# Kernel optimization log

Hardware: AMD Instinct MI355X
Metric: run time of the kernel (lower is better)

Reference implementation:

```python
import jax, jax.numpy as jnp
import numpy as np

N = 30000      # entities
E = 200000     # KG triples
E_ALL = 400000 # full-graph edges
R = 500        # relations
EH = 300       # e_hidden
RH = 100       # r_hidden
H = 8          # GAT / R2E heads
H_E2R = 2      # E2R heads: int(softmax(head_selector).sum()+1) == 2 always
EPS = 1e-16    # torch_geometric softmax eps


def _seg_softmax(logits, idx, num):
    # logits: [E, heads]; segment-wise stable softmax over edges grouped by idx
    m = jax.ops.segment_max(logits, idx, num_segments=num)
    ex = jnp.exp(logits - m[idx])
    s = jax.ops.segment_sum(ex, idx, num_segments=num)
    return ex / (s[idx] + EPS)


def _gcn(x, ei):
    j, i = ei[0], ei[1]
    deg = jax.ops.segment_sum(jnp.ones(ei.shape[1], x.dtype), i, num_segments=N)
    dis = jnp.where(deg > 0, deg ** -0.5, 0.0)
    norm = dis[j] * dis[i]                                        # [E_all]
    agg = jax.ops.segment_sum(norm[:, None] * x[j], i, num_segments=N)
    return jax.nn.relu(agg)


def _highway(x1, x2, w, b):
    gate = jax.nn.sigmoid(x1 @ w.T + b)
    return gate * x2 + (1.0 - gate) * x1


def setup_inputs() -> dict:
    key = jax.random.key(0)
    ks = jax.random.split(key, 20)
    f = jnp.float32
    inp = {
        'x_e': jax.random.normal(ks[0], (N, EH), f),
        'edge_index': jax.random.randint(ks[1], (2, E), 0, N),
        'rel': jax.random.randint(ks[2], (E,), 0, R),
        'edge_index_all': jax.random.randint(ks[3], (2, E_ALL), 0, N),
        'rel_all': jax.random.randint(ks[4], (E_ALL,), 0, R),
        # Highway layers
        'hw1_w': jax.random.normal(ks[5], (EH, EH), f) / np.sqrt(EH),
        'hw1_b': jnp.zeros((EH,), f),
        'hw2_w': jax.random.normal(ks[6], (EH, EH), f) / np.sqrt(EH),
        'hw2_b': jnp.zeros((EH,), f),
        # E2R (only first H_E2R heads are ever used)
        'e2r_wh': jax.random.normal(ks[7], (RH, EH), f) / np.sqrt(EH),
        'e2r_wt': jax.random.normal(ks[8], (RH, EH), f) / np.sqrt(EH),
        'e2r_ah': jax.random.normal(ks[9], (H_E2R, RH), f) / np.sqrt(RH),
        'e2r_at': jax.random.normal(ks[10], (H_E2R, RH), f) / np.sqrt(RH),
        # R2E
        'r2e_ah': jax.random.normal(ks[11], (H, EH), f) / np.sqrt(EH),
        'r2e_at': jax.random.normal(ks[12], (H, EH), f) / np.sqrt(EH),
        'r2e_ar': jax.random.normal(ks[13], (H, RH), f) / np.sqrt(RH),
        # GAT over e_hidden + 2*r_hidden = 500
        'gat_ai': jax.random.normal(ks[14], (H, EH + 2 * RH), f) / np.sqrt(EH + 2 * RH),
        'gat_aj': jax.random.normal(ks[15], (H, EH + 2 * RH), f) / np.sqrt(EH + 2 * RH),
    }
    return inp


def reference(x_e, edge_index, rel, edge_index_all, rel_all,
              hw1_w, hw1_b, hw2_w, hw2_b,
              e2r_wh, e2r_wt, e2r_ah, e2r_at,
              r2e_ah, r2e_at, r2e_ar, gat_ai, gat_aj):
    lrelu = jax.nn.leaky_relu  # slope 0.01, matches torch default

    # --- two GCN + Highway blocks (dropout = identity at eval) ---
    x = _highway(x_e, _gcn(x_e, edge_index_all), hw1_w, hw1_b)
    x = _highway(x, _gcn(x, edge_index_all), hw2_w, hw2_b)

    h_idx, t_idx = edge_index[0], edge_index[1]

    # --- E2R: entity -> relation (2 heads; spmm sum over heads folded into alpha sum) ---
    xh = x @ e2r_wh.T                        # [N, RH]
    xt = x @ e2r_wt.T                        # [N, RH]
    e1 = (xh @ e2r_ah.T)[h_idx] + (xt @ e2r_at.T)[t_idx]   # [E, H_E2R]
    a1 = _seg_softmax(lrelu(e1), rel, R)
    xr_h = jax.ops.segment_sum(a1.sum(1)[:, None] * xh[h_idx], rel, num_segments=R)
    e2 = (xt @ e2r_ah.T)[h_idx] + (xh @ e2r_at.T)[t_idx]
    a2 = _seg_softmax(lrelu(e2), rel, R)
    xr_t = jax.ops.segment_sum(a2.sum(1)[:, None] * xt[t_idx], rel, num_segments=R)
    x_r = (xr_h + xr_t) / H_E2R / 2.0        # [R, RH]

    # --- R2E: relation -> entity (8 heads) ---
    se_h = x @ r2e_ah.T                      # [N, H]
    se_t = x @ r2e_at.T
    sr = x_r @ r2e_ar.T                      # [R, H]
    a_h = _seg_softmax(lrelu(se_h[h_idx] + sr[rel]), h_idx, N)
    a_t = _seg_softmax(lrelu(se_t[t_idx] + sr[rel]), t_idx, N)
    xr_rel = x_r[rel]                        # [E, RH]
    xe_h = jax.ops.segment_sum(a_h.sum(1)[:, None] * xr_rel, h_idx, num_segments=N) / H
    xe_t = jax.ops.segment_sum(a_t.sum(1)[:, None] * xr_rel, t_idx, num_segments=N) / H
    x2 = jnp.concatenate([x, xe_h, xe_t], axis=1)          # [N, EH+2*RH]

    # --- GAT over full graph (8 heads) ---
    j_a, i_a = edge_index_all[0], edge_index_all[1]
    e_ij = (x2 @ gat_ai.T)[i_a] + (x2 @ gat_aj.T)[j_a]     # [E_all, H]
    al = _seg_softmax(lrelu(e_ij), i_a, N)
    x_gat = jax.ops.segment_sum(al.sum(1)[:, None] * x2[j_a], i_a, num_segments=N) / H

    return jnp.concatenate([x2, x_gat], axis=1)            # [N, 2*(EH+2*RH)]
```

## Files before the change

### kernel.cpp

```cpp
#include <hip/hip_runtime.h>
#include <math.h>

constexpr int N_    = 30000;
constexpr int E_    = 200000;
constexpr int EALL_ = 400000;
constexpr int R_    = 500;
constexpr int EH_   = 300;
constexpr int RH_   = 100;
constexpr int X2D_  = 500;
constexpr int OUTD_ = 1000;
constexpr int LD4   = OUTD_/4;
constexpr int EH4   = EH_/4;
constexpr int RH4   = RH_/4;
constexpr int NC_   = 16;
constexpr int XBS_  = 320;
constexpr int XEBS_ = 200;
constexpr int KP_   = 320;
constexpr int NBR_  = 64;
constexpr int PERB_ = (E_ + NBR_ - 1)/NBR_;

typedef __attribute__((ext_vector_type(4))) float f32x4;
typedef __attribute__((ext_vector_type(8))) short s16x8;

__device__ __forceinline__ float lrelu_(float v){ return v > 0.f ? v : 0.01f*v; }
__device__ __forceinline__ float sig_(float z){ return 1.f/(1.f + expf(-z)); }
__device__ __forceinline__ unsigned short f2bf_(float f){
  unsigned int u = __float_as_uint(f);
  unsigned int r = (u + 0x7FFFu + ((u >> 16) & 1u)) >> 16;
  return (unsigned short)r;
}
__device__ __forceinline__ float bf2f_(unsigned short h){
  return __uint_as_float(((unsigned int)h) << 16);
}

__global__ void k_count3(const int* __restrict__ ia,
                         const int* __restrict__ hi, const int* __restrict__ ti,
                         int* cd, int* ch, int* ct){
  int idx = blockIdx.x*blockDim.x + threadIdx.x;
  if (idx < EALL_) { atomicAdd(&cd[ia[idx]], 1); return; }
  idx -= EALL_;
  if (idx < E_) { atomicAdd(&ch[hi[idx]], 1); return; }
  idx -= E_;
  if (idx < E_) { atomicAdd(&ct[ti[idx]], 1); return; }
}

__global__ void k_scan3(const int* c0, int* o0, int L0,
                        const int* c1, int* o1, int L1,
                        const int* c2, int* o2, int L2,
                        float* __restrict__ dis){
  const int* c; int* o; int L;
  switch (blockIdx.x){
    case 0: c=c0; o=o0; L=L0; break;
    case 1: c=c1; o=o1; L=L1; break;
    default: c=c2; o=o2; L=L2; break;
  }
  __shared__ int sums[256];
  int t = threadIdx.x;
  int chunk = (L + 255) / 256;
  int s = min(t*chunk, L), e = min(s + chunk, L);
  int acc = 0;
  for (int i = s; i < e; ++i) acc += c[i];
  sums[t] = acc;
  __syncthreads();
  for (int off = 1; off < 256; off <<= 1) {
    int v = (t >= off) ? sums[t - off] : 0;
    __syncthreads();
    sums[t] += v;
    __syncthreads();
  }
  int run = t ? sums[t-1] : 0;
  for (int i = s; i < e; ++i) {
    o[i] = run; run += c[i];
    if (blockIdx.x == 0) dis[i] = (c[i] > 0) ? rsqrtf((float)c[i]) : 0.f;
  }
  if (t == 255) o[L] = sums[255];
}

__global__ void k_scatter3(const int* __restrict__ ja, const int* __restrict__ ia,
                           const int* __restrict__ rel, const int* __restrict__ hi,
                           const int* __restrict__ ti,
                           const int* od, const int* oh, const int* ot,
                           int* curd, int* curh, int* curt,
                           const float* __restrict__ dis,
                           int* j_dest, float* wj,
                           int* relh, int* relt){
  int idx = blockIdx.x*blockDim.x + threadIdx.x;
  if (idx < EALL_){
    int e = idx, s = ia[e];
    int p = od[s] + atomicAdd(&curd[s], 1);
    int j = ja[e];
    j_dest[p] = j; wj[p] = dis[j]; return;
  }
  idx -= EALL_;
  if (idx < E_){
    int e = idx, s = hi[e];
    int p = oh[s] + atomicAdd(&curh[s], 1);
    relh[p] = rel[e]; return;
  }
  idx -= E_;
  if (idx < E_){
    int e = idx, s = ti[e];
    int p = ot[s] + atomicAdd(&curt[s], 1);
    relt[p] = rel[e]; return;
  }
}

__global__ void k_relhist(const int* __restrict__ rel, int* __restrict__ H){
  __shared__ int h[R_];
  int b = blockIdx.x, tid = threadIdx.x;
  for (int i = tid; i < R_; i += 256) h[i] = 0;
  __syncthreads();
  int s = b*PERB_, e = min(s + PERB_, E_);
  for (int i = s + tid; i < e; i += 256) atomicAdd(&h[rel[i]], 1);
  __syncthreads();
  for (int i = tid; i < R_; i += 256) H[b*R_ + i] = h[i];
}

__global__ void k_relscan(int* __restrict__ H, int* __restrict__ off_rel){
  __shared__ int tot[R_];
  int tid = threadIdx.x;
  for (int r = tid; r < R_; r += 256){
    int acc = 0;
    for (int b = 0; b < NBR_; ++b){ int v = H[b*R_ + r]; H[b*R_ + r] = acc; acc += v; }
    tot[r] = acc;
  }
  __syncthreads();
  if (tid == 0){
    int run = 0;
    for (int r = 0; r < R_; ++r){ off_rel[r] = run; run += tot[r]; }
    off_rel[R_] = run;
  }
  __syncthreads();
  for (int r = tid; r < R_; r += 256){
    int o = off_rel[r];
    for (int b = 0; b < NBR_; ++b) H[b*R_ + r] += o;
  }
}

__global__ void k_relscatter(const int* __restrict__ rel, const int* __restrict__ hi,
                             const int* __restrict__ ti, const int* __restrict__ H,
                             int* __restrict__ hr, int* __restrict__ tr){
  __shared__ int cur[R_];
  int b = blockIdx.x, tid = threadIdx.x;
  for (int i = tid; i < R_; i += 256) cur[i] = H[b*R_ + i];
  __syncthreads();
  int s = b*PERB_, e = min(s + PERB_, E_);
  for (int i = s + tid; i < e; i += 256){
    int r = rel[i];
    int p = atomicAdd(&cur[r], 1);
    hr[p] = hi[i]; tr[p] = ti[i];
  }
}

__global__ void k_pack_x(const float4* __restrict__ X, int ldx4,
                         unsigned short* __restrict__ xb){
  int idx = blockIdx.x*blockDim.x + threadIdx.x;
  if (idx >= N_*80) return;
  int n = idx / 80, c = idx - n*80;
  ushort4 o = make_ushort4(0,0,0,0);
  if (c < EH4){
    float4 v = X[(size_t)n*ldx4 + c];
    o.x = f2bf_(v.x); o.y = f2bf_(v.y); o.z = f2bf_(v.z); o.w = f2bf_(v.w);
  }
  *reinterpret_cast<ushort4*>(&xb[(size_t)n*XBS_ + c*4]) = o;
}

__global__ void k_pack_w(const float* __restrict__ W, int Nn,
                         unsigned short* __restrict__ out){
  int idx = blockIdx.x*blockDim.x + threadIdx.x;
  if (idx >= Nn*KP_) return;
  int n = idx / KP_, k = idx - n*KP_;
  out[idx] = (k < EH_) ? f2bf_(W[(size_t)n*EH_ + k]) : (unsigned short)0;
}

__global__ void k_pack_wcat(const float* __restrict__ wh, const float* __restrict__ wt,
                            unsigned short* __restrict__ out){
  int idx = blockIdx.x*blockDim.x + threadIdx.x;
  if (idx >= 200*KP_) return;
  int n = idx / KP_, k = idx - n*KP_;
  unsigned short v = 0;
  if (k < EH_) v = f2bf_((n < 100) ? wh[(size_t)n*EH_ + k] : wt[(size_t)(n-100)*EH_ + k]);
  out[idx] = v;
}

__global__ __launch_bounds__(256) void k_gemm_mfma(
    const unsigned short* __restrict__ Ab,
    const unsigned short* __restrict__ Wb,
    float* __restrict__ C, int ldc, int M, int Nn){
  constexpr int WS = 328;
  constexpr int AS = 40;
  __shared__ unsigned short Ws[64*WS];
  __shared__ unsigned short As[128*AS];
  int tid = threadIdx.x;
  int lane = tid & 63, wave = tid >> 6;
  int wm = wave & 1, wn = wave >> 1;
  int m0 = blockIdx.x*128, n0 = blockIdx.y*64;

  for (int c = tid; c < 64*(KP_/8); c += 256){
    int n = c / (KP_/8), k8 = (c % (KP_/8))*8;
    s16x8 v = {0,0,0,0,0,0,0,0};
    if (n0 + n < Nn)
      v = *reinterpret_cast<const s16x8*>(&Wb[(size_t)(n0+n)*KP_ + k8]);
    *reinterpret_cast<s16x8*>(&Ws[n*WS + k8]) = v;
  }

  f32x4 acc[4][2] = {};
  int kf = (lane >> 4)*8;
  int rA = lane & 15;
  for (int k0 = 0; k0 < KP_; k0 += 32){
    __syncthreads();
    for (int c = tid; c < 128*4; c += 256){
      int r = c >> 2, k8 = (c & 3)*8;
      s16x8 v = {0,0,0,0,0,0,0,0};
      if (m0 + r < M)
        v = *reinterpret_cast<const s16x8*>(&Ab[(size_t)(m0+r)*XBS_ + k0 + k8]);
      *reinterpret_cast<s16x8*>(&As[r*AS + k8]) = v;
    }
    __syncthreads();
    s16x8 afr[4], bfr[2];
    #pragma unroll
    for (int mf = 0; mf < 4; ++mf)
      afr[mf] = *reinterpret_cast<const s16x8*>(&As[(wm*64 + mf*16 + rA)*AS + kf]);
    #pragma unroll
    for (int nf = 0; nf < 2; ++nf)
      bfr[nf] = *reinterpret_cast<const s16x8*>(&Ws[(wn*32 + nf*16 + rA)*WS + k0 + kf]);
    #pragma unroll
    for (int mf = 0; mf < 4; ++mf)
      #pragma unroll
      for (int nf = 0; nf < 2; ++nf)
        acc[mf][nf] = __builtin_amdgcn_mfma_f32_16x16x32_bf16(afr[mf], bfr[nf], acc[mf][nf], 0, 0, 0);
  }
  int col0 = n0 + wn*32 + (lane & 15);
  int rbase = m0 + wm*64 + (lane >> 4)*4;
  #pragma unroll
  for (int mf = 0; mf < 4; ++mf){
    #pragma unroll
    for (int nf = 0; nf < 2; ++nf){
      int col = col0 + nf*16;
      if (col < Nn){
        #pragma unroll
        for (int r = 0; r < 4; ++r){
          int row = rbase + mf*16 + r;
          if (row < M) C[(size_t)row*ldc + col] = acc[mf][nf][r];
        }
      }
    }
  }
}

__global__ void k_gcn4(const int* __restrict__ off, const int* __restrict__ jd,
                       const float* __restrict__ wj, const float* __restrict__ dis,
                       const unsigned short* __restrict__ xb, float4* __restrict__ Y){
  __shared__ int js[64];
  __shared__ float ws[64];
  int n = blockIdx.x, lane = threadIdx.x;
  int s = off[n], t = off[n+1];
  bool two = lane < (EH4 - 64);
  float4 a0 = make_float4(0.f,0.f,0.f,0.f);
  float4 a1 = make_float4(0.f,0.f,0.f,0.f);
  for (int base = s; base < t; base += 64){
    int m = min(64, t - base);
    __syncthreads();
    if (lane < m){ js[lane] = jd[base+lane]; ws[lane] = wj[base+lane]; }
    __syncthreads();
    int q = 0;
    for (; q + 1 < m; q += 2){
      size_t r0 = (size_t)js[q]*XBS_, r1 = (size_t)js[q+1]*XBS_;
      float w0 = ws[q], w1 = ws[q+1];
      ushort4 u0 = *reinterpret_cast<const ushort4*>(&xb[r0 + lane*4]);
      ushort4 u1 = *reinterpret_cast<const ushort4*>(&xb[r1 + lane*4]);
      a0.x += w0*bf2f_(u0.x) + w1*bf2f_(u1.x);
      a0.y += w0*bf2f_(u0.y) + w1*bf2f_(u1.y);
      a0.z += w0*bf2f_(u0.z) + w1*bf2f_(u1.z);
      a0.w += w0*bf2f_(u0.w) + w1*bf2f_(u1.w);
      if (two){
        ushort4 v0 = *reinterpret_cast<const ushort4*>(&xb[r0 + 256 + lane*4]);
        ushort4 v1 = *reinterpret_cast<const ushort4*>(&xb[r1 + 256 + lane*4]);
        a1.x += w0*bf2f_(v0.x) + w1*bf2f_(v1.x);
        a1.y += w0*bf2f_(v0.y) + w1*bf2f_(v1.y);
        a1.z += w0*bf2f_(v0.z) + w1*bf2f_(v1.z);
        a1.w += w0*bf2f_(v0.w) + w1*bf2f_(v1.w);
      }
    }
    if (q < m){
      size_t r0 = (size_t)js[q]*XBS_;
      float w0 = ws[q];
      ushort4 u0 = *reinterpret_cast<const ushort4*>(&xb[r0 + lane*4]);
      a0.x += w0*bf2f_(u0.x); a0.y += w0*bf2f_(u0.y);
      a0.z += w0*bf2f_(u0.z); a0.w += w0*bf2f_(u0.w);
      if (two){
        ushort4 v0 = *reinterpret_cast<const ushort4*>(&xb[r0 + 256 + lane*4]);
        a1.x += w0*bf2f_(v0.x); a1.y += w0*bf2f_(v0.y);
        a1.z += w0*bf2f_(v0.z); a1.w += w0*bf2f_(v0.w);
      }
    }
  }
  float dn = dis[n];
  float4 r;
  r.x = fmaxf(dn*a0.x, 0.f); r.y = fmaxf(dn*a0.y, 0.f);
  r.z = fmaxf(dn*a0.z, 0.f); r.w = fmaxf(dn*a0.w, 0.f);
  Y[(size_t)n*EH4 + lane] = r;
  if (two){
    r.x = fmaxf(dn*a1.x, 0.f); r.y = fmaxf(dn*a1.y, 0.f);
    r.z = fmaxf(dn*a1.z, 0.f); r.w = fmaxf(dn*a1.w, 0.f);
    Y[(size_t)n*EH4 + 64 + lane] = r;
  }
}

__global__ void k_highway3(const float4* __restrict__ Xold, int ldo4,
                           const float4* __restrict__ Y, const float4* __restrict__ G,
                           const float* __restrict__ b,
                           float4* __restrict__ Xn, unsigned short* __restrict__ xbb){
  int idx = blockIdx.x*blockDim.x + threadIdx.x;
  if (idx >= N_*EH4) return;
  int n = idx / EH4, f = idx - n*EH4;
  float4 g4 = G[idx];
  float4 b4 = reinterpret_cast<const float4*>(b)[f];
  float4 y4 = Y[idx];
  float4 xo = Xold[(size_t)n*ldo4 + f];
  float4 r;
  float gx;
  gx = sig_(g4.x + b4.x); r.x = gx*y4.x + (1.f-gx)*xo.x;
  gx = sig_(g4.y + b4.y); r.y = gx*y4.y + (1.f-gx)*xo.y;
  gx = sig_(g4.z + b4.z); r.z = gx*y4.z + (1.f-gx)*xo.z;
  gx = sig_(g4.w + b4.w); r.w = gx*y4.w + (1.f-gx)*xo.w;
  Xn[(size_t)n*LD4 + f] = r;
  ushort4 o;
  o.x = f2bf_(r.x); o.y = f2bf_(r.y); o.z = f2bf_(r.z); o.w = f2bf_(r.w);
  *reinterpret_cast<ushort4*>(&xbb[(size_t)n*XBS_ + f*4]) = o;
}

__global__ void k_pproj(const float* __restrict__ xhxt,
                        const float* __restrict__ ah, const float* __restrict__ at,
                        float4* __restrict__ pht){
  int n = blockIdx.x*blockDim.x + threadIdx.x;
  if (n >= N_) return;
  float a0=0,a1=0,b0=0,b1=0,c0=0,c1=0,d0=0,d1=0;
  const float* xh = xhxt + (size_t)n*200;
  const float* xt = xh + 100;
  for (int f = 0; f < RH_; ++f) {
    float vh = xh[f], vt = xt[f];
    float w0 = ah[f], w1 = ah[RH_+f], u0 = at[f], u1 = at[RH_+f];
    a0 += vh*w0; a1 += vh*w1;
    b0 += vt*u0; b1 += vt*u1;
    c0 += vt*w0; c1 += vt*w1;
    d0 += vh*u0; d1 += vh*u1;
  }
  pht[(size_t)n*2]     = make_float4(a0, a1, c0, c1);
  pht[(size_t)n*2 + 1] = make_float4(b0, b1, d0, d1);
}

__global__ void k_fold_rel2(const int* __restrict__ off,
                            const int* __restrict__ hr, const int* __restrict__ tr,
                            const float4* __restrict__ pht,
                            float* __restrict__ s1p, float* __restrict__ s2p){
  __shared__ float4 redm[4];
  __shared__ float4 reds[4];
  int r = blockIdx.x;
  int tid = threadIdx.x, lane = tid & 63, w = tid >> 6;
  int s = off[r], e = off[r+1];
  float4 mx = make_float4(-1e30f,-1e30f,-1e30f,-1e30f);
  for (int p = s + tid; p < e; p += 256){
    float4 ph = pht[(size_t)hr[p]*2];
    float4 pt = pht[(size_t)tr[p]*2 + 1];
    mx.x = fmaxf(mx.x, lrelu_(ph.x + pt.x));
    mx.y = fmaxf(mx.y, lrelu_(ph.y + pt.y));
    mx.z = fmaxf(mx.z, lrelu_(ph.z + pt.z));
    mx.w = fmaxf(mx.w, lrelu_(ph.w + pt.w));
  }
  #pragma unroll
  for (int o = 1; o < 64; o <<= 1){
    mx.x = fmaxf(mx.x, __shfl_xor(mx.x, o));
    mx.y = fmaxf(mx.y, __shfl_xor(mx.y, o));
    mx.z = fmaxf(mx.z, __shfl_xor(mx.z, o));
    mx.w = fmaxf(mx.w, __shfl_xor(mx.w, o));
  }
  if (lane == 0) redm[w] = mx;
  __syncthreads();
  float4 m;
  m.x = fmaxf(fmaxf(redm[0].x, redm[1].x), fmaxf(redm[2].x, redm[3].x));
  m.y = fmaxf(fmaxf(redm[0].y, redm[1].y), fmaxf(redm[2].y, redm[3].y));
  m.z = fmaxf(fmaxf(redm[0].z, redm[1].z), fmaxf(redm[2].z, redm[3].z));
  m.w = fmaxf(fmaxf(redm[0].w, redm[1].w), fmaxf(redm[2].w, redm[3].w));
  float4 sm = make_float4(0.f,0.f,0.f,0.f);
  for (int p = s + tid; p < e; p += 256){
    float4 ph = pht[(size_t)hr[p]*2];
    float4 pt = pht[(size_t)tr[p]*2 + 1];
    sm.x += expf(lrelu_(ph.x + pt.x) - m.x);
    sm.y += expf(lrelu_(ph.y + pt.y) - m.y);
    sm.z += expf(lrelu_(ph.z + pt.z) - m.z);
    sm.w += expf(lrelu_(ph.w + pt.w) - m.w);
  }
  #pragma unroll
  for (int o = 1; o < 64; o <<= 1){
    sm.x += __shfl_xor(sm.x, o);
    sm.y += __shfl_xor(sm.y, o);
    sm.z += __shfl_xor(sm.z, o);
    sm.w += __shfl_xor(sm.w, o);
  }
  if (lane == 0) reds[w] = sm;
  __syncthreads();
  float4 sv;
  sv.x = reds[0].x + reds[1].x + reds[2].x + reds[3].x;
  sv.y = reds[0].y + reds[1].y + reds[2].y + reds[3].y;
  sv.z = reds[0].z + reds[1].z + reds[2].z + reds[3].z;
  sv.w = reds[0].w + reds[1].w + reds[2].w + reds[3].w;
  float4 inv;
  inv.x = 1.f/(sv.x + 1e-16f); inv.y = 1.f/(sv.y + 1e-16f);
  inv.z = 1.f/(sv.z + 1e-16f); inv.w = 1.f/(sv.w + 1e-16f);
  for (int p = s + tid; p < e; p += 256){
    float4 ph = pht[(size_t)hr[p]*2];
    float4 pt = pht[(size_t)tr[p]*2 + 1];
    s1p[p] = expf(lrelu_(ph.x + pt.x) - m.x)*inv.x + expf(lrelu_(ph.y + pt.y) - m.y)*inv.y;
    s2p[p] = expf(lrelu_(ph.z + pt.z) - m.z)*inv.z + expf(lrelu_(ph.w + pt.w) - m.w)*inv.w;
  }
}

__global__ void k_fold_ht2(const int* __restrict__ offh, const int* __restrict__ offt,
                           const int* __restrict__ relh, const int* __restrict__ relt,
                           const float* __restrict__ st16, const float* __restrict__ sr8,
                           float* __restrict__ shp, float* __restrict__ stp){
  int w = threadIdx.x >> 6, lane = threadIdx.x & 63;
  int n = blockIdx.x*2 + (w >> 1);
  if (n >= N_) return;
  int side = w & 1;
  const int* off = side ? offt : offh;
  const int* rl  = side ? relt : relh;
  float* op = side ? stp : shp;
  int k = lane & 7, g = lane >> 3;
  float cst = st16[(size_t)n*16 + side*8 + k];
  int s = off[n], e = off[n+1];
  float m = -1e30f;
  for (int p = s + g; p < e; p += 8)
    m = fmaxf(m, lrelu_(cst + sr8[(size_t)rl[p]*8 + k]));
  #pragma unroll
  for (int o = 8; o < 64; o <<= 1) m = fmaxf(m, __shfl_xor(m, o));
  float sum = 0.f;
  for (int p = s + g; p < e; p += 8)
    sum += expf(lrelu_(cst + sr8[(size_t)rl[p]*8 + k]) - m);
  #pragma unroll
  for (int o = 8; o < 64; o <<= 1) sum += __shfl_xor(sum, o);
  float inv = 1.f / (sum + 1e-16f);
  for (int p = s + g; p < e; p += 8){
    float t = expf(lrelu_(cst + sr8[(size_t)rl[p]*8 + k]) - m) * inv;
    #pragma unroll
    for (int o = 1; o < 8; o <<= 1) t += __shfl_xor(t, o);
    if (k == 0) op[p] = t;
  }
}

__global__ void k_fold_gat2(const int* __restrict__ off, const int* __restrict__ jd,
                            const float* __restrict__ gg16, float* __restrict__ agp){
  int w = threadIdx.x >> 6, lane = threadIdx.x & 63;
  int n = blockIdx.x*4 + w;
  if (n >= N_) return;
  int k = lane & 7, g = lane >> 3;
  float cst = gg16[(size_t)n*16 + k];
  int s = off[n], e = off[n+1];
  float m = -1e30f;
  for (int p = s + g; p < e; p += 8)
    m = fmaxf(m, lrelu_(cst + gg16[(size_t)jd[p]*16 + 8 + k]));
  #pragma unroll
  for (int o = 8; o < 64; o <<= 1) m = fmaxf(m, __shfl_xor(m, o));
  float sum = 0.f;
  for (int p = s + g; p < e; p += 8)
    sum += expf(lrelu_(cst + gg16[(size_t)jd[p]*16 + 8 + k]) - m);
  #pragma unroll
  for (int o = 8; o < 64; o <<= 1) sum += __shfl_xor(sum, o);
  float inv = 1.f / (sum + 1e-16f);
  for (int p = s + g; p < e; p += 8){
    float t = expf(lrelu_(cst + gg16[(size_t)jd[p]*16 + 8 + k]) - m) * inv;
    #pragma unroll
    for (int o = 1; o < 8; o <<= 1) t += __shfl_xor(t, o);
    if (k == 0) agp[p] = t;
  }
}

__global__ void k_e2r_agg3(const int* __restrict__ off,
                           const int* __restrict__ hr, const int* __restrict__ tr,
                           const float* __restrict__ s1p, const float* __restrict__ s2p,
                           const float4* __restrict__ xhxt4, float4* __restrict__ xr_part){
  int r = blockIdx.x, c = blockIdx.y;
  int lane = threadIdx.x;
  int side = lane >> 5, fl = lane & 31;
  int s = off[r], e = off[r+1];
  int len = e - s;
  int per = (len + NC_ - 1)/NC_;
  int cs = s + c*per, ce = min(cs + per, e);
  float4 acc = make_float4(0.f,0.f,0.f,0.f);
  if (fl < RH4){
    const int* idx = side ? tr : hr;
    const float* wv = side ? s2p : s1p;
    int fofs = side ? 25 + fl : fl;
    int p = cs;
    for (; p + 1 < ce; p += 2){
      float a0 = wv[p], a1 = wv[p+1];
      float4 v0 = xhxt4[(size_t)idx[p]*50 + fofs];
      float4 v1 = xhxt4[(size_t)idx[p+1]*50 + fofs];
      acc.x += a0*v0.x + a1*v1.x; acc.y += a0*v0.y + a1*v1.y;
      acc.z += a0*v0.z + a1*v1.z; acc.w += a0*v0.w + a1*v1.w;
    }
    if (p < ce){
      float a0 = wv[p];
      float4 v0 = xhxt4[(size_t)idx[p]*50 + fofs];
      acc.x += a0*v0.x; acc.y += a0*v0.y; acc.z += a0*v0.z; acc.w += a0*v0.w;
    }
  }
  float4 oth;
  oth.x = __shfl_xor(acc.x, 32); oth.y = __shfl_xor(acc.y, 32);
  oth.z = __shfl_xor(acc.z, 32); oth.w = __shfl_xor(acc.w, 32);
  if (side == 0 && fl < RH4){
    float4 o = make_float4(acc.x+oth.x, acc.y+oth.y, acc.z+oth.z, acc.w+oth.w);
    xr_part[((size_t)c*R_ + r)*RH4 + fl] = o;
  }
}

__global__ void k_e2r_red(const float4* __restrict__ xr_part, float4* __restrict__ xr4){
  int idx = blockIdx.x*blockDim.x + threadIdx.x;
  if (idx >= R_*RH4) return;
  float4 a = make_float4(0.f,0.f,0.f,0.f);
  #pragma unroll
  for (int c = 0; c < NC_; ++c){
    float4 v = xr_part[(size_t)c*R_*RH4 + idx];
    a.x += v.x; a.y += v.y; a.z += v.z; a.w += v.w;
  }
  xr4[idx] = make_float4(a.x*0.25f, a.y*0.25f, a.z*0.25f, a.w*0.25f);
}

__global__ void k_dots16(const float* __restrict__ X, int ldx, int K,
                         const float* __restrict__ wA, const float* __restrict__ wB,
                         float* __restrict__ out16, int M){
  __shared__ float xs[16][65];
  __shared__ float ws[16][65];
  int tid = threadIdx.x;
  int tx = tid & 15, ty = tid >> 4;
  int r0 = blockIdx.x*16;
  float acc = 0.f;
  for (int c0 = 0; c0 < K; c0 += 64){
    int cl = min(64, K - c0);
    #pragma unroll
    for (int i = 0; i < 4; ++i){
      int idx = tid + i*256;
      int r = idx >> 6, k = idx & 63;
      float xv = 0.f, wv = 0.f;
      if (k < cl && r0 + r < M) xv = X[(size_t)(r0+r)*ldx + c0 + k];
      if (k < cl) wv = (r < 8) ? wA[(size_t)r*K + c0 + k] : wB[(size_t)(r-8)*K + c0 + k];
      xs[r][k] = xv;
      ws[r][k] = wv;
    }
    __syncthreads();
    #pragma unroll
    for (int k = 0; k < 64; ++k) acc += xs[ty][k]*ws[tx][k];
    __syncthreads();
  }
  if (r0 + ty < M) out16[(size_t)(r0+ty)*16 + tx] = acc;
}

__global__ void k_sr(const float* __restrict__ xr, const float* __restrict__ ar,
                     float* __restrict__ sr8){
  int idx = blockIdx.x*blockDim.x + threadIdx.x;
  if (idx >= R_*8) return;
  int r = idx >> 3, h = idx & 7;
  float acc = 0.f;
  for (int k = 0; k < RH_; ++k) acc += xr[(size_t)r*RH_ + k]*ar[(size_t)h*RH_ + k];
  sr8[idx] = acc;
}

__global__ void k_r2e_agg2b(const int* __restrict__ offh, const int* __restrict__ offt,
                            const int* __restrict__ relh, const int* __restrict__ relt,
                            const float* __restrict__ shp, const float* __restrict__ stp,
                            const float4* __restrict__ xr4, float4* __restrict__ out,
                            unsigned short* __restrict__ xeb){
  int n = blockIdx.x;
  int side = threadIdx.x >> 6, lane = threadIdx.x & 63;
  const int* off = side ? offt : offh;
  const int* rr  = side ? relt : relh;
  const float* sp = side ? stp : shp;
  int s = off[n], e = off[n+1];
  if (lane >= RH4) return;
  float4 acc = make_float4(0.f,0.f,0.f,0.f);
  int p = s;
  for (; p + 1 < e; p += 2){
    float a0 = sp[p], a1 = sp[p+1];
    float4 v0 = xr4[(size_t)rr[p]*RH4 + lane];
    float4 v1 = xr4[(size_t)rr[p+1]*RH4 + lane];
    acc.x += a0*v0.x + a1*v1.x; acc.y += a0*v0.y + a1*v1.y;
    acc.z += a0*v0.z + a1*v1.z; acc.w += a0*v0.w + a1*v1.w;
  }
  if (p < e){
    float a0 = sp[p];
    float4 v0 = xr4[(size_t)rr[p]*RH4 + lane];
    acc.x += a0*v0.x; acc.y += a0*v0.y; acc.z += a0*v0.z; acc.w += a0*v0.w;
  }
  float4 o = make_float4(acc.x*0.125f, acc.y*0.125f, acc.z*0.125f, acc.w*0.125f);
  out[(size_t)n*LD4 + (side ? 100 : 75) + lane] = o;
  ushort4 ob;
  ob.x = f2bf_(o.x); ob.y = f2bf_(o.y); ob.z = f2bf_(o.z); ob.w = f2bf_(o.w);
  *reinterpret_cast<ushort4*>(&xeb[(size_t)n*XEBS_ + (side ? 100 : 0) + lane*4]) = ob;
}

__global__ void k_gat_agg4(const int* __restrict__ off, const int* __restrict__ jd,
                           const float* __restrict__ agp,
                           const unsigned short* __restrict__ xb,
                           const unsigned short* __restrict__ xeb,
                           float4* __restrict__ out){
  __shared__ int js[128];
  __shared__ float as_[128];
  int n = blockIdx.x, tid = threadIdx.x;
  int s = off[n], t = off[n+1];
  const unsigned short* tbl;
  size_t stride; int cofs;
  if (tid < 75){ tbl = xb;  stride = XBS_;  cofs = tid*4; }
  else         { tbl = xeb; stride = XEBS_; cofs = (tid-75)*4; }
  float4 acc = make_float4(0.f,0.f,0.f,0.f);
  for (int base = s; base < t; base += 128){
    int m = min(128, t - base);
    __syncthreads();
    if (tid < m){ js[tid] = jd[base+tid]; as_[tid] = agp[base+tid]; }
    __syncthreads();
    if (tid < 125){
      int q = 0;
      for (; q + 1 < m; q += 2){
        float a0 = as_[q], a1 = as_[q+1];
        ushort4 u0 = *reinterpret_cast<const ushort4*>(&tbl[(size_t)js[q]*stride + cofs]);
        ushort4 u1 = *reinterpret_cast<const ushort4*>(&tbl[(size_t)js[q+1]*stride + cofs]);
        acc.x += a0*bf2f_(u0.x) + a1*bf2f_(u1.x);
        acc.y += a0*bf2f_(u0.y) + a1*bf2f_(u1.y);
        acc.z += a0*bf2f_(u0.z) + a1*bf2f_(u1.z);
        acc.w += a0*bf2f_(u0.w) + a1*bf2f_(u1.w);
      }
      if (q < m){
        float a0 = as_[q];
        ushort4 u0 = *reinterpret_cast<const ushort4*>(&tbl[(size_t)js[q]*stride + cofs]);
        acc.x += a0*bf2f_(u0.x); acc.y += a0*bf2f_(u0.y);
        acc.z += a0*bf2f_(u0.z); acc.w += a0*bf2f_(u0.w);
      }
    }
  }
  if (tid < 125){
    float4 r = make_float4(acc.x*0.125f, acc.y*0.125f, acc.z*0.125f, acc.w*0.125f);
    out[(size_t)n*LD4 + 125 + tid] = r;
  }
}

static inline void gemm_mfma(const unsigned short* Ab, const unsigned short* Wb,
                             float* C, int ldc, int M, int Nn, hipStream_t st){
  dim3 g((M + 127)/128, (Nn + 63)/64);
  k_gemm_mfma<<<g, 256, 0, st>>>(Ab, Wb, C, ldc, M, Nn);
}

extern "C" void kernel_launch(void* const* d_in, const int* in_sizes, int n_in,
                              void* d_out, int out_size, void* d_ws, size_t ws_size,
                              hipStream_t stream) {
  const float* x_e   = (const float*)d_in[0];
  const int*   ei    = (const int*)d_in[1];
  const int*   rel   = (const int*)d_in[2];
  const int*   eia   = (const int*)d_in[3];
  const float* hw1_w = (const float*)d_in[5];
  const float* hw1_b = (const float*)d_in[6];
  const float* hw2_w = (const float*)d_in[7];
  const float* hw2_b = (const float*)d_in[8];
  const float* e2r_wh= (const float*)d_in[9];
  const float* e2r_wt= (const float*)d_in[10];
  const float* e2r_ah= (const float*)d_in[11];
  const float* e2r_at= (const float*)d_in[12];
  const float* r2e_ah= (const float*)d_in[13];
  const float* r2e_at= (const float*)d_in[14];
  const float* r2e_ar= (const float*)d_in[15];
  const float* gat_ai= (const float*)d_in[16];
  const float* gat_aj= (const float*)d_in[17];
  float* out = (float*)d_out;

  const int* hi = ei;
  const int* ti = ei + E_;
  const int* ja = eia;
  const int* ia = eia + EALL_;

  char* base = (char*)d_ws;
  size_t off = 0;
  auto alloc = [&](size_t bytes)->void*{
    void* p = base + off;
    off = (off + bytes + 255) & ~(size_t)255;
    return p;
  };

  size_t z0 = off;
  int* cnt_dest = (int*)alloc(N_*4);
  int* cur_dest = (int*)alloc(N_*4);
  int* cnt_h    = (int*)alloc(N_*4);
  int* cur_h    = (int*)alloc(N_*4);
  int* cnt_t    = (int*)alloc(N_*4);
  int* cur_t    = (int*)alloc(N_*4);
  size_t z1 = off;

  int* off_dest = (int*)alloc((N_+1)*4);
  int* off_rel  = (int*)alloc((R_+1)*4);
  int* off_h    = (int*)alloc((N_+1)*4);
  int* off_t    = (int*)alloc((N_+1)*4);
  int* Hrel     = (int*)alloc((size_t)NBR_*R_*4);
  int* j_dest   = (int*)alloc((size_t)EALL_*4);
  int* hr       = (int*)alloc((size_t)E_*4);
  int* tr       = (int*)alloc((size_t)E_*4);
  int* relh     = (int*)alloc((size_t)E_*4);
  int* relt     = (int*)alloc((size_t)E_*4);

  float* dis   = (float*)alloc(N_*4);
  float* wj    = (float*)alloc((size_t)EALL_*4);
  float* y     = (float*)alloc((size_t)N_*EH_*4);
  float* g     = (float*)alloc((size_t)N_*EH_*4);
  float* xhxt  = (float*)alloc((size_t)N_*200*4);
  float* pht   = (float*)alloc((size_t)N_*8*4);
  float* s1p   = (float*)alloc((size_t)E_*4);
  float* s2p   = (float*)alloc((size_t)E_*4);
  float* xr    = (float*)alloc((size_t)R_*RH_*4);
  float* xr_part=(float*)alloc((size_t)NC_*R_*RH_*4);
  float* st16  = (float*)alloc((size_t)N_*16*4);
  float* sr8   = (float*)alloc((size_t)R_*8*4);
  float* shp   = (float*)alloc((size_t)E_*4);
  float* stp   = (float*)alloc((size_t)E_*4);
  float* gg16  = (float*)alloc((size_t)N_*16*4);
  float* agp   = (float*)alloc((size_t)EALL_*4);
  unsigned short* xb  = (unsigned short*)alloc((size_t)N_*XBS_*2);
  unsigned short* xeb = (unsigned short*)alloc((size_t)N_*XEBS_*2);
  unsigned short* w1b = (unsigned short*)alloc((size_t)EH_*KP_*2);
  unsigned short* w2b = (unsigned short*)alloc((size_t)EH_*KP_*2);
  unsigned short* wcb = (unsigned short*)alloc((size_t)200*KP_*2);

  hipMemsetAsync(base + z0, 0, z1 - z0, stream);

  const int TB = 256;
  const int TOT = EALL_ + 2*E_;
  int gTOT  = (TOT + TB - 1)/TB;
  int gN    = (N_ + TB - 1)/TB;
  int gPKX  = (N_*80 + TB - 1)/TB;

  k_pack_w<<<(EH_*KP_ + TB - 1)/TB, TB, 0, stream>>>(hw1_w, EH_, w1b);
  k_pack_w<<<(EH_*KP_ + TB - 1)/TB, TB, 0, stream>>>(hw2_w, EH_, w2b);
  k_pack_wcat<<<(200*KP_ + TB - 1)/TB, TB, 0, stream>>>(e2r_wh, e2r_wt, wcb);

  k_relhist<<<NBR_, 256, 0, stream>>>(rel, Hrel);
  k_relscan<<<1, 256, 0, stream>>>(Hrel, off_rel);
  k_relscatter<<<NBR_, 256, 0, stream>>>(rel, hi, ti, Hrel, hr, tr);

  k_count3<<<gTOT, TB, 0, stream>>>(ia, hi, ti, cnt_dest, cnt_h, cnt_t);
  k_scan3<<<3, 256, 0, stream>>>(cnt_dest, off_dest, N_, cnt_h, off_h, N_, cnt_t, off_t, N_, dis);
  k_scatter3<<<gTOT, TB, 0, stream>>>(ja, ia, rel, hi, ti,
                                      off_dest, off_h, off_t,
                                      cur_dest, cur_h, cur_t,
                                      dis, j_dest, wj, relh, relt);

  k_pack_x<<<gPKX, TB, 0, stream>>>((const float4*)x_e, EH4, xb);
  gemm_mfma(xb, w1b, g, EH_, N_, EH_, stream);
  k_gcn4<<<N_, 64, 0, stream>>>(off_dest, j_dest, wj, dis, xb, (float4*)y);
  k_highway3<<<(N_*EH4 + TB - 1)/TB, TB, 0, stream>>>((const float4*)x_e, EH4, (const float4*)y,
                                                      (const float4*)g, hw1_b, (float4*)out, xb);
  gemm_mfma(xb, w2b, g, EH_, N_, EH_, stream);
  k_gcn4<<<N_, 64, 0, stream>>>(off_dest, j_dest, wj, dis, xb, (float4*)y);
  k_highway3<<<(N_*EH4 + TB - 1)/TB, TB, 0, stream>>>((const float4*)out, LD4, (const float4*)y,
                                                      (const float4*)g, hw2_b, (float4*)out, xb);

  gemm_mfma(xb, wcb, xhxt, 200, N_, 200, stream);
  k_pproj<<<gN, TB, 0, stream>>>(xhxt, e2r_ah, e2r_at, (float4*)pht);
  k_fold_rel2<<<R_, 256, 0, stream>>>(off_rel, hr, tr, (const float4*)pht, s1p, s2p);
  k_e2r_agg3<<<dim3(R_, NC_), 64, 0, stream>>>(off_rel, hr, tr, s1p, s2p,
                                               (const float4*)xhxt, (float4*)xr_part);
  k_e2r_red<<<(R_*RH4 + TB - 1)/TB, TB, 0, stream>>>((const float4*)xr_part, (float4*)xr);

  k_dots16<<<(N_+15)/16, 256, 0, stream>>>(out, OUTD_, EH_, r2e_ah, r2e_at, st16, N_);
  k_sr<<<(R_*8 + TB - 1)/TB, TB, 0, stream>>>(xr, r2e_ar, sr8);
  k_fold_ht2<<<(N_+1)/2, 256, 0, stream>>>(off_h, off_t, relh, relt, st16, sr8, shp, stp);
  k_r2e_agg2b<<<N_, 128, 0, stream>>>(off_h, off_t, relh, relt, shp, stp,
                                      (const float4*)xr, (float4*)out, xeb);

  k_dots16<<<(N_+15)/16, 256, 0, stream>>>(out, OUTD_, X2D_, gat_ai, gat_aj, gg16, N_);
  k_fold_gat2<<<(N_+3)/4, 256, 0, stream>>>(off_dest, j_dest, gg16, agp);
  k_gat_agg4<<<N_, 128, 0, stream>>>(off_dest, j_dest, agp, xb, xeb, (float4*)out);
}
```

Baseline: 718.2 us.

## Parallelize CSR prefix scans and merge small weight-pack and relation-score kernels

Replaces the three-block serial prefix scan over node counts with a multi-block three-phase scan (block sums, tiny sum scan, per-block scan), which pads the count and offset arrays to a multiple of the scan block size. The relation offset scan becomes a parallel shared-memory scan instead of a single-thread loop. The three weight-packing kernels are merged into one launch, and the relation score computation is folded into the E2R reduction kernel. Together these are meant to cut serialized setup time and launch count. The cost is extra launches for the scan phases and larger padded buffers.

```diff
diff --git a/kernel.cpp b/kernel.cpp
--- a/kernel.cpp
+++ b/kernel.cpp
@@ -18,6 +18,9 @@
 constexpr int KP_   = 320;
 constexpr int NBR_  = 64;
 constexpr int PERB_ = (E_ + NBR_ - 1)/NBR_;
+constexpr int SCB_  = 2048;
+constexpr int NSB_  = (N_ + SCB_ - 1)/SCB_;
+constexpr int SCNP_ = NSB_*SCB_;
 
 typedef __attribute__((ext_vector_type(4))) float f32x4;
 typedef __attribute__((ext_vector_type(8))) short s16x8;
@@ -44,36 +47,63 @@
   if (idx < E_) { atomicAdd(&ct[ti[idx]], 1); return; }
 }
 
-__global__ void k_scan3(const int* c0, int* o0, int L0,
-                        const int* c1, int* o1, int L1,
-                        const int* c2, int* o2, int L2,
-                        float* __restrict__ dis){
-  const int* c; int* o; int L;
-  switch (blockIdx.x){
-    case 0: c=c0; o=o0; L=L0; break;
-    case 1: c=c1; o=o1; L=L1; break;
-    default: c=c2; o=o2; L=L2; break;
-  }
-  __shared__ int sums[256];
+__global__ void k_scanA(const int* __restrict__ c0, const int* __restrict__ c1,
+                        const int* __restrict__ c2, int* __restrict__ bsum){
+  int arr = blockIdx.x / NSB_, b = blockIdx.x - arr*NSB_;
+  const int* c = arr == 0 ? c0 : (arr == 1 ? c1 : c2);
   int t = threadIdx.x;
-  int chunk = (L + 255) / 256;
-  int s = min(t*chunk, L), e = min(s + chunk, L);
-  int acc = 0;
-  for (int i = s; i < e; ++i) acc += c[i];
-  sums[t] = acc;
-  __syncthreads();
-  for (int off = 1; off < 256; off <<= 1) {
-    int v = (t >= off) ? sums[t - off] : 0;
-    __syncthreads();
-    sums[t] += v;
-    __syncthreads();
-  }
-  int run = t ? sums[t-1] : 0;
-  for (int i = s; i < e; ++i) {
-    o[i] = run; run += c[i];
-    if (blockIdx.x == 0) dis[i] = (c[i] > 0) ? rsqrtf((float)c[i]) : 0.f;
-  }
-  if (t == 255) o[L] = sums[255];
+  const int4* c4 = reinterpret_cast<const int4*>(c + b*SCB_ + t*8);
+  int4 u0 = c4[0], u1 = c4[1];
+  int acc = u0.x+u0.y+u0.z+u0.w + u1.x+u1.y+u1.z+u1.w;
+  __shared__ int red[256];
+  red[t] = acc;
+  __syncthreads();
+  for (int o = 128; o > 0; o >>= 1){
+    if (t < o) red[t] += red[t+o];
+    __syncthreads();
+  }
+  if (t == 0) bsum[arr*NSB_ + b] = red[0];
+}
+
+__global__ void k_scanB(int* __restrict__ bsum, int* o0, int* o1, int* o2){
+  int t = threadIdx.x;
+  if (t < 3){
+    int run = 0;
+    for (int b = 0; b < NSB_; ++b){ int v = bsum[t*NSB_ + b]; bsum[t*NSB_ + b] = run; run += v; }
+    int* o = t == 0 ? o0 : (t == 1 ? o1 : o2);
+    o[N_] = run;
+  }
+}
+
+__global__ void k_scanC(const int* __restrict__ c0, const int* __restrict__ c1,
+                        const int* __restrict__ c2, const int* __restrict__ bsum,
+                        int* o0, int* o1, int* o2, float* __restrict__ dis){
+  int arr = blockIdx.x / NSB_, b = blockIdx.x - arr*NSB_;
+  const int* c = arr == 0 ? c0 : (arr == 1 ? c1 : c2);
+  int* o = arr == 0 ? o0 : (arr == 1 ? o1 : o2);
+  int t = threadIdx.x;
+  int base = b*SCB_ + t*8;
+  const int4* c4 = reinterpret_cast<const int4*>(c + base);
+  int4 u0 = c4[0], u1 = c4[1];
+  int v[8] = {u0.x,u0.y,u0.z,u0.w,u1.x,u1.y,u1.z,u1.w};
+  int tot = v[0]+v[1]+v[2]+v[3]+v[4]+v[5]+v[6]+v[7];
+  __shared__ int sc[256];
+  sc[t] = tot;
+  __syncthreads();
+  for (int off = 1; off < 256; off <<= 1){
+    int add = (t >= off) ? sc[t-off] : 0;
+    __syncthreads();
+    sc[t] += add;
+    __syncthreads();
+  }
+  int run = bsum[arr*NSB_ + b] + (t ? sc[t-1] : 0);
+  #pragma unroll
+  for (int i = 0; i < 8; ++i){
+    int idx = base + i;
+    o[idx] = run;
+    if (arr == 0) dis[idx] = v[i] > 0 ? rsqrtf((float)v[i]) : 0.f;
+    run += v[i];
+  }
 }
 
 __global__ void k_scatter3(const int* __restrict__ ja, const int* __restrict__ ia,
@@ -118,6 +148,7 @@
 
 __global__ void k_relscan(int* __restrict__ H, int* __restrict__ off_rel){
   __shared__ int tot[R_];
+  __shared__ int sc[256];
   int tid = threadIdx.x;
   for (int r = tid; r < R_; r += 256){
     int acc = 0;
@@ -125,11 +156,21 @@
     tot[r] = acc;
   }
   __syncthreads();
-  if (tid == 0){
-    int run = 0;
-    for (int r = 0; r < R_; ++r){ off_rel[r] = run; run += tot[r]; }
-    off_rel[R_] = run;
-  }
+  int r0 = tid*2;
+  int a0 = (r0 < R_) ? tot[r0] : 0;
+  int a1 = (r0+1 < R_) ? tot[r0+1] : 0;
+  sc[tid] = a0 + a1;
+  __syncthreads();
+  for (int off = 1; off < 256; off <<= 1){
+    int add = (tid >= off) ? sc[tid-off] : 0;
+    __syncthreads();
+    sc[tid] += add;
+    __syncthreads();
+  }
+  int run = tid ? sc[tid-1] : 0;
+  if (r0 < R_)   off_rel[r0]   = run;
+  if (r0+1 < R_) off_rel[r0+1] = run + a0;
+  if (tid == 255) off_rel[R_] = sc[255];
   __syncthreads();
   for (int r = tid; r < R_; r += 256){
     int o = off_rel[r];
@@ -165,22 +206,28 @@
   *reinterpret_cast<ushort4*>(&xb[(size_t)n*XBS_ + c*4]) = o;
 }
 
-__global__ void k_pack_w(const float* __restrict__ W, int Nn,
-                         unsigned short* __restrict__ out){
+__global__ void k_pack_weights(const float* __restrict__ w1, const float* __restrict__ w2,
+                               const float* __restrict__ wh, const float* __restrict__ wt,
+                               unsigned short* w1b, unsigned short* w2b,
+                               unsigned short* wcb){
   int idx = blockIdx.x*blockDim.x + threadIdx.x;
-  if (idx >= Nn*KP_) return;
-  int n = idx / KP_, k = idx - n*KP_;
-  out[idx] = (k < EH_) ? f2bf_(W[(size_t)n*EH_ + k]) : (unsigned short)0;
-}
-
-__global__ void k_pack_wcat(const float* __restrict__ wh, const float* __restrict__ wt,
-                            unsigned short* __restrict__ out){
-  int idx = blockIdx.x*blockDim.x + threadIdx.x;
-  if (idx >= 200*KP_) return;
-  int n = idx / KP_, k = idx - n*KP_;
-  unsigned short v = 0;
-  if (k < EH_) v = f2bf_((n < 100) ? wh[(size_t)n*EH_ + k] : wt[(size_t)(n-100)*EH_ + k]);
-  out[idx] = v;
+  if (idx < EH_*KP_){
+    int n = idx/KP_, k = idx - n*KP_;
+    w1b[idx] = (k < EH_) ? f2bf_(w1[(size_t)n*EH_ + k]) : (unsigned short)0;
+    return;
+  }
+  idx -= EH_*KP_;
+  if (idx < EH_*KP_){
+    int n = idx/KP_, k = idx - n*KP_;
+    w2b[idx] = (k < EH_) ? f2bf_(w2[(size_t)n*EH_ + k]) : (unsigned short)0;
+    return;
+  }
+  idx -= EH_*KP_;
+  if (idx < 200*KP_){
+    int n = idx/KP_, k = idx - n*KP_;
+    wcb[idx] = (k < EH_) ? f2bf_((n < 100) ? wh[(size_t)n*EH_ + k] : wt[(size_t)(n-100)*EH_ + k])
+                         : (unsigned short)0;
+  }
 }
 
 __global__ __launch_bounds__(256) void k_gemm_mfma(
@@ -515,16 +562,29 @@
   }
 }
 
-__global__ void k_e2r_red(const float4* __restrict__ xr_part, float4* __restrict__ xr4){
-  int idx = blockIdx.x*blockDim.x + threadIdx.x;
-  if (idx >= R_*RH4) return;
-  float4 a = make_float4(0.f,0.f,0.f,0.f);
+__global__ void k_e2r_red2(const float4* __restrict__ xr_part, float4* __restrict__ xr4,
+                           const float* __restrict__ ar, float* __restrict__ sr8){
+  __shared__ float row[RH_];
+  int r = blockIdx.x, lane = threadIdx.x;
+  if (lane < RH4){
+    float4 a = make_float4(0.f,0.f,0.f,0.f);
+    #pragma unroll
+    for (int c = 0; c < NC_; ++c){
+      float4 v = xr_part[((size_t)c*R_ + r)*RH4 + lane];
+      a.x += v.x; a.y += v.y; a.z += v.z; a.w += v.w;
+    }
+    a.x *= 0.25f; a.y *= 0.25f; a.z *= 0.25f; a.w *= 0.25f;
+    xr4[(size_t)r*RH4 + lane] = a;
+    row[lane*4]   = a.x; row[lane*4+1] = a.y;
+    row[lane*4+2] = a.z; row[lane*4+3] = a.w;
+  }
+  __syncthreads();
+  int h = lane & 7, gk = lane >> 3;
+  float acc = 0.f;
+  for (int k = gk; k < RH_; k += 8) acc += row[k]*ar[(size_t)h*RH_ + k];
   #pragma unroll
-  for (int c = 0; c < NC_; ++c){
-    float4 v = xr_part[(size_t)c*R_*RH4 + idx];
-    a.x += v.x; a.y += v.y; a.z += v.z; a.w += v.w;
-  }
-  xr4[idx] = make_float4(a.x*0.25f, a.y*0.25f, a.z*0.25f, a.w*0.25f);
+  for (int o = 8; o < 64; o <<= 1) acc += __shfl_xor(acc, o);
+  if (lane < 8) sr8[(size_t)r*8 + lane] = acc;
 }
 
 __global__ void k_dots16(const float* __restrict__ X, int ldx, int K,
@@ -556,16 +616,6 @@
   if (r0 + ty < M) out16[(size_t)(r0+ty)*16 + tx] = acc;
 }
 
-__global__ void k_sr(const float* __restrict__ xr, const float* __restrict__ ar,
-                     float* __restrict__ sr8){
-  int idx = blockIdx.x*blockDim.x + threadIdx.x;
-  if (idx >= R_*8) return;
-  int r = idx >> 3, h = idx & 7;
-  float acc = 0.f;
-  for (int k = 0; k < RH_; ++k) acc += xr[(size_t)r*RH_ + k]*ar[(size_t)h*RH_ + k];
-  sr8[idx] = acc;
-}
-
 __global__ void k_r2e_agg2b(const int* __restrict__ offh, const int* __restrict__ offt,
                             const int* __restrict__ relh, const int* __restrict__ relt,
                             const float* __restrict__ shp, const float* __restrict__ stp,
@@ -685,18 +735,19 @@
   };
 
   size_t z0 = off;
-  int* cnt_dest = (int*)alloc(N_*4);
+  int* cnt_dest = (int*)alloc(SCNP_*4);
+  int* cnt_h    = (int*)alloc(SCNP_*4);
+  int* cnt_t    = (int*)alloc(SCNP_*4);
   int* cur_dest = (int*)alloc(N_*4);
-  int* cnt_h    = (int*)alloc(N_*4);
   int* cur_h    = (int*)alloc(N_*4);
-  int* cnt_t    = (int*)alloc(N_*4);
   int* cur_t    = (int*)alloc(N_*4);
   size_t z1 = off;
 
-  int* off_dest = (int*)alloc((N_+1)*4);
+  int* off_dest = (int*)alloc(SCNP_*4);
+  int* off_h    = (int*)alloc(SCNP_*4);
+  int* off_t    = (int*)alloc(SCNP_*4);
   int* off_rel  = (int*)alloc((R_+1)*4);
-  int* off_h    = (int*)alloc((N_+1)*4);
-  int* off_t    = (int*)alloc((N_+1)*4);
+  int* bsum     = (int*)alloc(3*NSB_*4);
   int* Hrel     = (int*)alloc((size_t)NBR_*R_*4);
   int* j_dest   = (int*)alloc((size_t)EALL_*4);
   int* hr       = (int*)alloc((size_t)E_*4);
@@ -704,7 +755,7 @@
   int* relh     = (int*)alloc((size_t)E_*4);
   int* relt     = (int*)alloc((size_t)E_*4);
 
-  float* dis   = (float*)alloc(N_*4);
+  float* dis   = (float*)alloc(SCNP_*4);
   float* wj    = (float*)alloc((size_t)EALL_*4);
   float* y     = (float*)alloc((size_t)N_*EH_*4);
   float* g     = (float*)alloc((size_t)N_*EH_*4);
@@ -733,17 +784,20 @@
   int gTOT  = (TOT + TB - 1)/TB;
   int gN    = (N_ + TB - 1)/TB;
   int gPKX  = (N_*80 + TB - 1)/TB;
-
-  k_pack_w<<<(EH_*KP_ + TB - 1)/TB, TB, 0, stream>>>(hw1_w, EH_, w1b);
-  k_pack_w<<<(EH_*KP_ + TB - 1)/TB, TB, 0, stream>>>(hw2_w, EH_, w2b);
-  k_pack_wcat<<<(200*KP_ + TB - 1)/TB, TB, 0, stream>>>(e2r_wh, e2r_wt, wcb);
+  const int WTOT = 2*EH_*KP_ + 200*KP_;
+
+  k_pack_weights<<<(WTOT + TB - 1)/TB, TB, 0, stream>>>(hw1_w, hw2_w, e2r_wh, e2r_wt,
+                                                        w1b, w2b, wcb);
 
   k_relhist<<<NBR_, 256, 0, stream>>>(rel, Hrel);
   k_relscan<<<1, 256, 0, stream>>>(Hrel, off_rel);
   k_relscatter<<<NBR_, 256, 0, stream>>>(rel, hi, ti, Hrel, hr, tr);
 
   k_count3<<<gTOT, TB, 0, stream>>>(ia, hi, ti, cnt_dest, cnt_h, cnt_t);
-  k_scan3<<<3, 256, 0, stream>>>(cnt_dest, off_dest, N_, cnt_h, off_h, N_, cnt_t, off_t, N_, dis);
+  k_scanA<<<3*NSB_, 256, 0, stream>>>(cnt_dest, cnt_h, cnt_t, bsum);
+  k_scanB<<<1, 64, 0, stream>>>(bsum, off_dest, off_h, off_t);
+  k_scanC<<<3*NSB_, 256, 0, stream>>>(cnt_dest, cnt_h, cnt_t, bsum,
+                                      off_dest, off_h, off_t, dis);
   k_scatter3<<<gTOT, TB, 0, stream>>>(ja, ia, rel, hi, ti,
                                       off_dest, off_h, off_t,
                                       cur_dest, cur_h, cur_t,
@@ -764,10 +818,9 @@
   k_fold_rel2<<<R_, 256, 0, stream>>>(off_rel, hr, tr, (const float4*)pht, s1p, s2p);
   k_e2r_agg3<<<dim3(R_, NC_), 64, 0, stream>>>(off_rel, hr, tr, s1p, s2p,
                                                (const float4*)xhxt, (float4*)xr_part);
-  k_e2r_red<<<(R_*RH4 + TB - 1)/TB, TB, 0, stream>>>((const float4*)xr_part, (float4*)xr);
+  k_e2r_red2<<<R_, 64, 0, stream>>>((const float4*)xr_part, (float4*)xr, r2e_ar, sr8);
 
   k_dots16<<<(N_+15)/16, 256, 0, stream>>>(out, OUTD_, EH_, r2e_ah, r2e_at, st16, N_);
-  k_sr<<<(R_*8 + TB - 1)/TB, TB, 0, stream>>>(xr, r2e_ar, sr8);
   k_fold_ht2<<<(N_+1)/2, 256, 0, stream>>>(off_h, off_t, relh, relt, st16, sr8, shp, stp);
   k_r2e_agg2b<<<N_, 128, 0, stream>>>(off_h, off_t, relh, relt, shp, stp,
                                       (const float4*)xr, (float4*)out, xeb);
```

Result: faster. 651.8 us (-9.3%).
